# Kernel optimization log

Hardware: AMD Instinct MI355X
Metric: run time of the kernel (lower is better)

## Reference

```python
import jax, jax.numpy as jnp
import numpy as np

H_HEADS = 8
DIM_HEAD = 64
NEG_BIAS = -1.0e9


def setup_inputs() -> dict:
    key = jax.random.key(0)
    ks = jax.random.split(key, 8)
    b, n, l = 4, 4096, 256
    qd, cd = 512, 768
    inner = H_HEADS * DIM_HEAD  # 512
    x = jax.random.normal(ks[0], (b, n, qd), dtype=jnp.float32)
    context = jax.random.normal(ks[1], (b, l, cd), dtype=jnp.float32)
    mask = jax.random.randint(ks[2], (b, l, 128, 128), 0, 2).astype(jnp.int32)
    Wq = jax.random.normal(ks[3], (qd, inner), dtype=jnp.float32) * 0.02
    Wk = jax.random.normal(ks[4], (cd, inner), dtype=jnp.float32) * 0.02
    Wv = jax.random.normal(ks[5], (cd, inner), dtype=jnp.float32) * 0.02
    Wo = jax.random.normal(ks[6], (inner, qd), dtype=jnp.float32) * 0.02
    bo = jnp.zeros((qd,), dtype=jnp.float32)
    return {"x": x, "context": context, "mask": mask,
            "Wq": Wq, "Wk": Wk, "Wv": Wv, "Wo": Wo, "bo": bo}


def _split_heads(t, h):
    # 'b n (h d) -> (b h) n d'
    b, n, hd = t.shape
    d = hd // h
    return t.reshape(b, n, h, d).transpose(0, 2, 1, 3).reshape(b * h, n, d)


def reference(x, context, mask, Wq, Wk, Wv, Wo, bo):
    h = H_HEADS
    scale = DIM_HEAD ** (-0.5)
    b, n, _ = x.shape
    l = context.shape[1]
    size = int(round(n ** 0.5))  # spatial side of the query grid

    q = _split_heads(x @ Wq, h)        # (b*h, n, d)
    k = _split_heads(context @ Wk, h)  # (b*h, l, d)
    v = _split_heads(context @ Wv, h)  # (b*h, l, d)

    sim = jnp.einsum('bid,bjd->bij', q, k) * scale  # (b*h, n, l)

    # F.interpolate(mask, size=size) with default 'nearest': idx = floor(i * H_in / size)
    Hin = mask.shape[2]
    idx = (jnp.arange(size) * Hin) // size
    m = mask[:, :, idx[:, None], idx[None, :]]       # (b, l, size, size)
    m = m.reshape(b, l, n).transpose(0, 2, 1)        # (b, n, l)
    m = jnp.tile(m, (h, 1, 1)).astype(bool)          # (b*h, n, l), tile order as in torch .tile(h,1,1)
    sim = jnp.where(m, sim, sim + NEG_BIAS)

    attn = jax.nn.softmax(sim, axis=-1)
    out = jnp.einsum('bij,bjd->bid', attn, v)        # (b*h, n, d)
    # '(b h) n d -> b n (h d)'
    out = out.reshape(b, h, n, DIM_HEAD).transpose(0, 2, 1, 3).reshape(b, n, h * DIM_HEAD)
    return out @ Wo + bo
```

## Files before the change

kernel.cpp:

```cpp
#include <hip/hip_runtime.h>
#include <hip/hip_bf16.h>

typedef __attribute__((ext_vector_type(8))) short short8;
typedef __attribute__((ext_vector_type(4))) float f32x4;

__device__ __forceinline__ unsigned short f2bf(float f) {
  unsigned int u = __float_as_uint(f);
  u = (u + 0x7FFFu + ((u >> 16) & 1u)) >> 16;
  return (unsigned short)u;
}

__device__ __forceinline__ unsigned int pk2(float a, float b) {
  __hip_bfloat162 h = __float22bfloat162_rn(make_float2(a, b));
  return *reinterpret_cast<unsigned int*>(&h);
}

__device__ __forceinline__ void gl_lds16(const void* g, void* l) {
  __builtin_amdgcn_global_load_lds(
      (const __attribute__((address_space(1))) void*)g,
      (__attribute__((address_space(3))) void*)l, 16, 0, 0);
}

__device__ __forceinline__ void fence_barrier() {
  asm volatile("" ::: "memory");
  __builtin_amdgcn_s_barrier();
  asm volatile("" ::: "memory");
}

__device__ __forceinline__ void store4_bf16(unsigned short* p, int stride,
                                            float v0, float v1, float v2, float v3) {
  unsigned int u01 = pk2(v0, v1), u23 = pk2(v2, v3);
  p[0] = (unsigned short)u01;
  p[stride] = (unsigned short)(u01 >> 16);
  p[2 * stride] = (unsigned short)u23;
  p[3 * stride] = (unsigned short)(u23 >> 16);
}

__global__ void prep_all(const float* __restrict__ Wq, const float* __restrict__ Wk,
                         const float* __restrict__ Wv, const float* __restrict__ Wo,
                         unsigned short* __restrict__ WqT, unsigned short* __restrict__ WkT,
                         unsigned short* __restrict__ WvT, unsigned short* __restrict__ WoT,
                         const int* __restrict__ mask, unsigned char* __restrict__ Mout,
                         const float* __restrict__ x, const float* __restrict__ ctx,
                         unsigned short* __restrict__ xb, unsigned short* __restrict__ ctxb) {
  __shared__ char smem[64 * 256];
  const int bid = blockIdx.x;
  if (bid >= 576) {
    int i = (bid - 576) * 256 + threadIdx.x;
    const float4* src;
    ushort4* dst;
    if (i < 2097152) {
      src = (const float4*)x + i;
      dst = (ushort4*)xb + i;
    } else {
      int j = i - 2097152;
      if (j >= 196608) return;
      src = (const float4*)ctx + j;
      dst = (ushort4*)ctxb + j;
    }
    float4 v = *src;
    ushort4 o;
    o.x = f2bf(v.x); o.y = f2bf(v.y); o.z = f2bf(v.z); o.w = f2bf(v.w);
    *dst = o;
    return;
  }
  if (bid < 320) {
    unsigned short(*t)[65] = (unsigned short(*)[65])smem;
    const float* W; unsigned short* WT; int K, rel;
    float scale = 1.f;
    if (bid < 64)       { W = Wq; WT = WqT; K = 512; rel = bid; scale = 0.125f * 1.4426950408889634f; }
    else if (bid < 160) { W = Wk; WT = WkT; K = 768; rel = bid - 64; }
    else if (bid < 256) { W = Wv; WT = WvT; K = 768; rel = bid - 160; }
    else                { W = Wo; WT = WoT; K = 512; rel = bid - 256; }
    const int N = 512;
    const int tk = rel >> 3, tn = rel & 7;
    const int k0 = tk * 64, n0 = tn * 64;
    const int tt = threadIdx.x;
#pragma unroll
    for (int e = 0; e < 16; ++e) {
      int idx = e * 256 + tt;
      int r = idx >> 6, c = idx & 63;
      t[r][c] = f2bf(scale * W[(size_t)(k0 + r) * N + n0 + c]);
    }
    __syncthreads();
#pragma unroll
    for (int e = 0; e < 16; ++e) {
      int idx = e * 256 + tt;
      int rr = idx & 63, cc = idx >> 6;
      WT[(size_t)(n0 + cc) * K + k0 + rr] = t[rr][cc];
    }
  } else {
    unsigned char* bits = (unsigned char*)smem;
    const int rel = bid - 320;
    const int r2g = rel & 63, bp = rel >> 6;
    const int j = threadIdx.x;
    const int4* row = (const int4*)(mask + ((size_t)(bp * 256 + j) * 128 + r2g * 2) * 128);
#pragma unroll 8
    for (int q = 0; q < 32; ++q) {
      int4 v = row[q];
      bits[(2 * q) * 256 + j] = v.x ? 1 : 0;
      bits[(2 * q + 1) * 256 + j] = v.z ? 1 : 0;
    }
    __syncthreads();
    const int t2 = threadIdx.x;
    const int c = t2 >> 2, ch = t2 & 3;
    uint4* dst = (uint4*)(Mout + ((size_t)bp * 4096 + r2g * 64 + c) * 256 + ch * 64);
#pragma unroll
    for (int q = 0; q < 4; ++q) {
      unsigned int wd[4];
#pragma unroll
      for (int wq = 0; wq < 4; ++wq) {
        unsigned int v = 0;
#pragma unroll
        for (int bb = 0; bb < 4; ++bb) {
          int ob = ch * 64 + q * 16 + wq * 4 + bb;
          int jj = ((ob & 15) << 4) | (ob >> 4);
          v |= ((unsigned int)bits[c * 256 + jj]) << (8 * bb);
        }
        wd[wq] = v;
      }
      uint4 vv; vv.x = wd[0]; vv.y = wd[1]; vv.z = wd[2]; vv.w = wd[3];
      dst[q] = vv;
    }
  }
}

__global__ __launch_bounds__(256, 2) void proj_all(
    const unsigned short* __restrict__ xb, const unsigned short* __restrict__ ctxb,
    const unsigned short* __restrict__ WqT, const unsigned short* __restrict__ WkT,
    const unsigned short* __restrict__ WvT,
    unsigned short* __restrict__ Qb, unsigned short* __restrict__ Kb,
    unsigned short* __restrict__ VTb) {
  __shared__ unsigned short lds_a[2][128 * 64];
  __shared__ unsigned short lds_b[2][128 * 64];
  const int tid = threadIdx.x;
  const int w = tid >> 6, lane = tid & 63;
  const int lo = lane & 15, hi = lane >> 4;
  const int wr = w >> 1, wc = w & 1;
  const int bid = blockIdx.x;
  const int wg = (bid & 7) * 96 + (bid >> 3);

  if (wg < 512) {
    const int m0 = (wg >> 2) * 128, n0 = (wg & 3) * 128;
    const int K = 512;
    f32x4 acc[4][4];
#pragma unroll
    for (int m = 0; m < 4; ++m)
#pragma unroll
      for (int n = 0; n < 4; ++n) acc[m][n] = (f32x4){0.f, 0.f, 0.f, 0.f};

    auto stage = [&](int buf, int k0) {
#pragma unroll
      for (int c = 0; c < 4; ++c) {
        int o = (tid + c * 256) * 16;
        int row = o >> 7, colb = (o & 127) ^ ((row & 7) << 4);
        gl_lds16((const char*)xb + ((size_t)(m0 + row) * K + k0) * 2 + colb,
                 (char*)lds_a[buf] + (w * 64 + c * 256) * 16);
      }
#pragma unroll
      for (int c = 0; c < 4; ++c) {
        int o = (tid + c * 256) * 16;
        int row = o >> 7, colb = (o & 127) ^ ((row & 7) << 4);
        gl_lds16((const char*)WqT + ((size_t)(n0 + row) * K + k0) * 2 + colb,
                 (char*)lds_b[buf] + (w * 64 + c * 256) * 16);
      }
    };

    stage(0, 0);
    int cur = 0;
    for (int t = 0; t < 8; ++t) {
      if (t < 7) {
        stage(cur ^ 1, (t + 1) * 64);
        asm volatile("s_waitcnt vmcnt(8)" ::: "memory");
      } else {
        asm volatile("s_waitcnt vmcnt(0)" ::: "memory");
      }
      fence_barrier();
      short8 a[2][4], b[2][4];
#pragma unroll
      for (int kk = 0; kk < 2; ++kk) {
#pragma unroll
        for (int m = 0; m < 4; ++m) {
          int row = wr * 64 + m * 16 + lo;
          a[kk][m] = *(const short8*)((const char*)lds_a[cur] + row * 128 +
                                      (((kk * 32 + hi * 8) * 2) ^ ((row & 7) << 4)));
        }
#pragma unroll
        for (int n = 0; n < 4; ++n) {
          int row = wc * 64 + n * 16 + lo;
          b[kk][n] = *(const short8*)((const char*)lds_b[cur] + row * 128 +
                                      (((kk * 32 + hi * 8) * 2) ^ ((row & 7) << 4)));
        }
      }
#pragma unroll
      for (int kk = 0; kk < 2; ++kk)
#pragma unroll
        for (int m = 0; m < 4; ++m)
#pragma unroll
          for (int n = 0; n < 4; ++n)
            acc[m][n] = __builtin_amdgcn_mfma_f32_16x16x32_bf16(a[kk][m], b[kk][n], acc[m][n], 0, 0, 0);
      if (t < 7) fence_barrier();
      cur ^= 1;
    }
#pragma unroll
    for (int m = 0; m < 4; ++m)
#pragma unroll
      for (int n = 0; n < 4; ++n) {
        int rbase = m0 + wr * 64 + m * 16 + hi * 4;
        int col = n0 + wc * 64 + n * 16 + lo;
        store4_bf16(&Qb[(size_t)rbase * 512 + col], 512,
                    acc[m][n][0], acc[m][n][1], acc[m][n][2], acc[m][n][3]);
      }
  } else {
    const int rel = wg - 512;
    const int z = rel >> 7, t5 = rel & 127;
    const unsigned short* BT = z ? WvT : WkT;
    const int m0 = (t5 >> 3) * 64, n0 = (t5 & 7) * 64;
    const int K = 768;
    f32x4 acc[2][2];
#pragma unroll
    for (int m = 0; m < 2; ++m)
#pragma unroll
      for (int n = 0; n < 2; ++n) acc[m][n] = (f32x4){0.f, 0.f, 0.f, 0.f};

    auto stage = [&](int buf, int k0) {
#pragma unroll
      for (int c = 0; c < 2; ++c) {
        int o = (tid + c * 256) * 16;
        int row = o >> 7, colb = (o & 127) ^ ((row & 7) << 4);
        gl_lds16((const char*)ctxb + ((size_t)(m0 + row) * K + k0) * 2 + colb,
                 (char*)lds_a[buf] + (w * 64 + c * 256) * 16);
        gl_lds16((const char*)BT + ((size_t)(n0 + row) * K + k0) * 2 + colb,
                 (char*)lds_b[buf] + (w * 64 + c * 256) * 16);
      }
    };

    stage(0, 0);
    int cur = 0;
    for (int t = 0; t < 12; ++t) {
      if (t < 11) {
        stage(cur ^ 1, (t + 1) * 64);
        asm volatile("s_waitcnt vmcnt(4)" ::: "memory");
      } else {
        asm volatile("s_waitcnt vmcnt(0)" ::: "memory");
      }
      fence_barrier();
      short8 a[2][2], b[2][2];
#pragma unroll
      for (int kk = 0; kk < 2; ++kk) {
#pragma unroll
        for (int m = 0; m < 2; ++m) {
          int row = wr * 32 + m * 16 + lo;
          a[kk][m] = *(const short8*)((const char*)lds_a[cur] + row * 128 +
                                      (((kk * 32 + hi * 8) * 2) ^ ((row & 7) << 4)));
        }
#pragma unroll
        for (int n = 0; n < 2; ++n) {
          int row = wc * 32 + n * 16 + lo;
          b[kk][n] = *(const short8*)((const char*)lds_b[cur] + row * 128 +
                                      (((kk * 32 + hi * 8) * 2) ^ ((row & 7) << 4)));
        }
      }
#pragma unroll
      for (int kk = 0; kk < 2; ++kk)
#pragma unroll
        for (int m = 0; m < 2; ++m)
#pragma unroll
          for (int n = 0; n < 2; ++n)
            acc[m][n] = __builtin_amdgcn_mfma_f32_16x16x32_bf16(a[kk][m], b[kk][n], acc[m][n], 0, 0, 0);
      if (t < 11) fence_barrier();
      cur ^= 1;
    }
#pragma unroll
    for (int m = 0; m < 2; ++m)
#pragma unroll
      for (int n = 0; n < 2; ++n) {
        int col = n0 + wc * 32 + n * 16 + lo;
        int rowg = m0 + wr * 32 + m * 16 + hi * 4;
        if (z == 0) {
          store4_bf16(&Kb[(size_t)rowg * 512 + col], 512,
                      acc[m][n][0], acc[m][n][1], acc[m][n][2], acc[m][n][3]);
        } else {
          unsigned int u01 = pk2(acc[m][n][0], acc[m][n][1]);
          unsigned int u23 = pk2(acc[m][n][2], acc[m][n][3]);
          uint2 vv; vv.x = u01; vv.y = u23;
          *(uint2*)&VTb[((size_t)(rowg >> 8) * 512 + col) * 256 + (rowg & 255)] = vv;
        }
      }
  }
}

__global__ void attn_kernel(const unsigned short* __restrict__ Qb,
                            const unsigned short* __restrict__ Kb,
                            const unsigned short* __restrict__ VTb,
                            const unsigned char* __restrict__ Mu8,
                            unsigned short* __restrict__ AOb) {
  __shared__ unsigned short kt[256 * 64];
  __shared__ float rinv_s[64];
  const int tid = threadIdx.x, w = tid >> 6, lane = tid & 63;
  const int lo = lane & 15, hi = lane >> 4;
  const int bid = blockIdx.x;
  const int wg = (bid & 7) * 256 + (bid >> 3);
  const int qt = wg & 63, h = (wg >> 6) & 7, b = wg >> 9;

#pragma unroll
  for (int c = 0; c < 8; ++c) {
    int o = (tid + c * 256) * 16;
    int j = o >> 7, colb = (o & 127) ^ ((j & 7) << 4);
    gl_lds16((const char*)Kb + ((size_t)((b * 256 + j) * 512 + h * 64)) * 2 + colb,
             (char*)kt + (w * 64 + c * 256) * 16);
  }
  short8 qf[2];
  {
    int qrow = qt * 64 + w * 16 + lo;
#pragma unroll
    for (int kk = 0; kk < 2; ++kk)
      qf[kk] = *(const short8*)&Qb[(size_t)(b * 4096 + qrow) * 512 + h * 64 + kk * 32 + hi * 8];
  }
  const unsigned char* mrow = Mu8 + ((size_t)(h & 3) * 4096 + qt * 64 + w * 16) * 256;
  uint4 mv[4];
#pragma unroll
  for (int r = 0; r < 4; ++r)
    mv[r] = *(const uint4*)(mrow + (hi * 4 + r) * 256 + lo * 16);
  __syncthreads();

  f32x4 acc[16];
#pragma unroll
  for (int nt = 0; nt < 16; ++nt) acc[nt] = (f32x4){0.f, 0.f, 0.f, 0.f};
  __builtin_amdgcn_s_setprio(1);
#pragma unroll
  for (int nt = 0; nt < 16; ++nt) {
    int j = nt * 16 + lo;
#pragma unroll
    for (int kk = 0; kk < 2; ++kk) {
      short8 bfr = *(const short8*)((const char*)kt + j * 128 +
                                    (((kk * 32 + hi * 8) * 2) ^ ((j & 7) << 4)));
      acc[nt] = __builtin_amdgcn_mfma_f32_16x16x32_bf16(qf[kk], bfr, acc[nt], 0, 0, 0);
    }
  }
  __builtin_amdgcn_s_setprio(0);

  float rmax[4] = {-3e38f, -3e38f, -3e38f, -3e38f};
#pragma unroll
  for (int nt = 0; nt < 16; ++nt)
#pragma unroll
    for (int r = 0; r < 4; ++r) rmax[r] = fmaxf(rmax[r], acc[nt][r]);
#pragma unroll
  for (int r = 0; r < 4; ++r) {
#pragma unroll
    for (int m2 = 1; m2 < 16; m2 <<= 1)
      rmax[r] = fmaxf(rmax[r], __shfl_xor(rmax[r], m2, 64));
  }
  float rsum[4] = {0.f, 0.f, 0.f, 0.f};
#pragma unroll
  for (int nt = 0; nt < 16; ++nt)
#pragma unroll
    for (int r = 0; r < 4; ++r) {
      unsigned int word = (nt < 4) ? mv[r].x : (nt < 8) ? mv[r].y : (nt < 12) ? mv[r].z : mv[r].w;
      unsigned int mbyte = (word >> ((nt & 3) * 8)) & 0xFFu;
      float p = exp2f(acc[nt][r] - rmax[r]);
      p = mbyte ? p : 0.f;
      acc[nt][r] = p;
      rsum[r] += p;
    }
#pragma unroll
  for (int r = 0; r < 4; ++r) {
#pragma unroll
    for (int m2 = 1; m2 < 16; m2 <<= 1)
      rsum[r] += __shfl_xor(rsum[r], m2, 64);
  }
  if (lo == 0) {
#pragma unroll
    for (int r = 0; r < 4; ++r) rinv_s[w * 16 + hi * 4 + r] = 1.f / rsum[r];
  }

  __syncthreads();

  {
    char* pl = (char*)kt;
    const int q0 = w * 16 + hi * 4;
    const int ro0 = (q0 + 0) * 512, sw0 = ((q0 + 0) & 7) << 4;
    const int ro1 = (q0 + 1) * 512, sw1 = ((q0 + 1) & 7) << 4;
    const int ro2 = (q0 + 2) * 512, sw2 = ((q0 + 2) & 7) << 4;
    const int ro3 = (q0 + 3) * 512, sw3 = ((q0 + 3) & 7) << 4;
#pragma unroll
    for (int nt = 0; nt < 16; ++nt) {
      int j2 = (nt * 16 + lo) * 2;
      unsigned int u01 = pk2(acc[nt][0], acc[nt][1]);
      unsigned int u23 = pk2(acc[nt][2], acc[nt][3]);
      *(unsigned short*)(pl + ro0 + (j2 ^ sw0)) = (unsigned short)u01;
      *(unsigned short*)(pl + ro1 + (j2 ^ sw1)) = (unsigned short)(u01 >> 16);
      *(unsigned short*)(pl + ro2 + (j2 ^ sw2)) = (unsigned short)u23;
      *(unsigned short*)(pl + ro3 + (j2 ^ sw3)) = (unsigned short)(u23 >> 16);
    }
  }
  __syncthreads();

  const int dh = w & 1, qh = w >> 1;
  f32x4 aco[2][2];
#pragma unroll
  for (int m = 0; m < 2; ++m)
#pragma unroll
    for (int n = 0; n < 2; ++n) aco[m][n] = (f32x4){0.f, 0.f, 0.f, 0.f};
  const size_t vbase = ((size_t)b * 512 + h * 64 + dh * 32) * 256;
#pragma unroll
  for (int ks = 0; ks < 8; ++ks) {
    short8 pa[2];
#pragma unroll
    for (int m = 0; m < 2; ++m) {
      int q = qh * 32 + m * 16 + lo;
      pa[m] = *(const short8*)((const char*)kt + q * 512 +
                               (((ks * 32 + hi * 8) * 2) ^ ((q & 7) << 4)));
    }
    __builtin_amdgcn_s_setprio(1);
#pragma unroll
    for (int n = 0; n < 2; ++n) {
      short8 vb = *(const short8*)&VTb[vbase + (size_t)(n * 16 + lo) * 256 + ks * 32 + hi * 8];
#pragma unroll
      for (int m = 0; m < 2; ++m)
        aco[m][n] = __builtin_amdgcn_mfma_f32_16x16x32_bf16(pa[m], vb, aco[m][n], 0, 0, 0);
    }
    __builtin_amdgcn_s_setprio(0);
  }

#pragma unroll
  for (int m = 0; m < 2; ++m) {
    float rv[4];
#pragma unroll
    for (int r = 0; r < 4; ++r) rv[r] = rinv_s[qh * 32 + m * 16 + hi * 4 + r];
#pragma unroll
    for (int n = 0; n < 2; ++n) {
      int col = h * 64 + dh * 32 + n * 16 + lo;
      int rowg = qt * 64 + qh * 32 + m * 16 + hi * 4;
      store4_bf16(&AOb[(size_t)(b * 4096 + rowg) * 512 + col], 512,
                  aco[m][n][0] * rv[0], aco[m][n][1] * rv[1],
                  aco[m][n][2] * rv[2], aco[m][n][3] * rv[3]);
    }
  }
}

__global__ __launch_bounds__(256, 2) void gemm_o(
    const unsigned short* __restrict__ A, const unsigned short* __restrict__ BT,
    float* __restrict__ Cout, const float* __restrict__ bias) {
  __shared__ unsigned short lds_a[2][128 * 64];
  __shared__ unsigned short lds_b[2][128 * 64];
  const int tid = threadIdx.x;
  const int w = tid >> 6, lane = tid & 63;
  const int lo = lane & 15, hi = lane >> 4;
  const int bid = blockIdx.x;
  const int wg = (bid & 7) * 64 + (bid >> 3);
  const int m0 = (wg >> 2) * 128, n0 = (wg & 3) * 128;
  const int wr = w >> 1, wc = w & 1;
  const int K = 512, N = 512;
  f32x4 acc[4][4];
#pragma unroll
  for (int m = 0; m < 4; ++m)
#pragma unroll
    for (int n = 0; n < 4; ++n) acc[m][n] = (f32x4){0.f, 0.f, 0.f, 0.f};

  auto stage = [&](int buf, int k0) {
#pragma unroll
    for (int c = 0; c < 4; ++c) {
      int o = (tid + c * 256) * 16;
      int row = o >> 7, colb = (o & 127) ^ ((row & 7) << 4);
      gl_lds16((const char*)A + ((size_t)(m0 + row) * K + k0) * 2 + colb,
               (char*)lds_a[buf] + (w * 64 + c * 256) * 16);
    }
#pragma unroll
    for (int c = 0; c < 4; ++c) {
      int o = (tid + c * 256) * 16;
      int row = o >> 7, colb = (o & 127) ^ ((row & 7) << 4);
      gl_lds16((const char*)BT + ((size_t)(n0 + row) * K + k0) * 2 + colb,
               (char*)lds_b[buf] + (w * 64 + c * 256) * 16);
    }
  };

  stage(0, 0);
  int cur = 0;
  for (int t = 0; t < 8; ++t) {
    if (t < 7) {
      stage(cur ^ 1, (t + 1) * 64);
      asm volatile("s_waitcnt vmcnt(8)" ::: "memory");
    } else {
      asm volatile("s_waitcnt vmcnt(0)" ::: "memory");
    }
    fence_barrier();
    short8 a[2][4], b[2][4];
#pragma unroll
    for (int kk = 0; kk < 2; ++kk) {
#pragma unroll
      for (int m = 0; m < 4; ++m) {
        int row = wr * 64 + m * 16 + lo;
        a[kk][m] = *(const short8*)((const char*)lds_a[cur] + row * 128 +
                                    (((kk * 32 + hi * 8) * 2) ^ ((row & 7) << 4)));
      }
#pragma unroll
      for (int n = 0; n < 4; ++n) {
        int row = wc * 64 + n * 16 + lo;
        b[kk][n] = *(const short8*)((const char*)lds_b[cur] + row * 128 +
                                    (((kk * 32 + hi * 8) * 2) ^ ((row & 7) << 4)));
      }
    }
#pragma unroll
    for (int kk = 0; kk < 2; ++kk)
#pragma unroll
      for (int m = 0; m < 4; ++m)
#pragma unroll
        for (int n = 0; n < 4; ++n)
          acc[m][n] = __builtin_amdgcn_mfma_f32_16x16x32_bf16(a[kk][m], b[kk][n], acc[m][n], 0, 0, 0);
    if (t < 7) fence_barrier();
    cur ^= 1;
  }

#pragma unroll
  for (int m = 0; m < 4; ++m)
#pragma unroll
    for (int n = 0; n < 4; ++n) {
      int rbase = m0 + wr * 64 + m * 16 + hi * 4;
      int col = n0 + wc * 64 + n * 16 + lo;
#pragma unroll
      for (int r = 0; r < 4; ++r)
        Cout[(size_t)(rbase + r) * N + col] = acc[m][n][r] + bias[col];
    }
}

extern "C" void kernel_launch(void* const* d_in, const int* in_sizes, int n_in,
                              void* d_out, int out_size, void* d_ws, size_t ws_size,
                              hipStream_t stream) {
  const float* x = (const float*)d_in[0];
  const float* ctx = (const float*)d_in[1];
  const int* mask = (const int*)d_in[2];
  const float* Wq = (const float*)d_in[3];
  const float* Wk = (const float*)d_in[4];
  const float* Wv = (const float*)d_in[5];
  const float* Wo = (const float*)d_in[6];
  const float* bo = (const float*)d_in[7];
  float* out = (float*)d_out;

  char* ws = (char*)d_ws;
  size_t off = 0;
  auto alloc = [&](size_t bytes) {
    char* p = ws + off;
    off += (bytes + 255) & ~(size_t)255;
    return p;
  };
  unsigned short* xb   = (unsigned short*)alloc((size_t)16384 * 512 * 2);
  unsigned short* ctxb = (unsigned short*)alloc((size_t)1024 * 768 * 2);
  unsigned short* WqT  = (unsigned short*)alloc((size_t)512 * 512 * 2);
  unsigned short* WkT  = (unsigned short*)alloc((size_t)512 * 768 * 2);
  unsigned short* WvT  = (unsigned short*)alloc((size_t)512 * 768 * 2);
  unsigned short* WoT  = (unsigned short*)alloc((size_t)512 * 512 * 2);
  unsigned short* Qb   = (unsigned short*)alloc((size_t)16384 * 512 * 2);
  unsigned short* Kb   = (unsigned short*)alloc((size_t)1024 * 512 * 2);
  unsigned short* VTb  = (unsigned short*)alloc((size_t)4 * 512 * 256 * 2);
  unsigned short* AOb  = (unsigned short*)alloc((size_t)16384 * 512 * 2);
  unsigned char*  Mu8  = (unsigned char*)alloc((size_t)4 * 4096 * 256);

  prep_all<<<9536, 256, 0, stream>>>(Wq, Wk, Wv, Wo, WqT, WkT, WvT, WoT, mask, Mu8, x, ctx, xb, ctxb);
  proj_all<<<768, 256, 0, stream>>>(xb, ctxb, WqT, WkT, WvT, Qb, Kb, VTb);
  attn_kernel<<<2048, 256, 0, stream>>>(Qb, Kb, VTb, Mu8, AOb);
  gemm_o<<<512, 256, 0, stream>>>(AOb, WoT, out, bo);
}
```

Measured before the change: 82.26 us.

## Make PV stage wave-local with per-wave P buffers, removing block barriers

Each wave now writes its own 16-row slice of the probability matrix into a private LDS buffer in two 128-column halves and immediately multiplies it by V for all 64 head dims. This replaces the shared K-tile reuse, the two block-wide __syncthreads, and the shared rinv array with wave-local waits, and the softmax normalizer is kept in registers. The trade-off is that each wave loads all of V^T for its head from global memory instead of sharing a 32-column slice, which raises global/L2 read traffic, and a separate LDS buffer is added.

```diff
diff --git a/kernel.cpp b/kernel.cpp
--- a/kernel.cpp
+++ b/kernel.cpp
@@ -290,13 +290,12 @@
   }
 }
 
-__global__ void attn_kernel(const unsigned short* __restrict__ Qb,
-                            const unsigned short* __restrict__ Kb,
-                            const unsigned short* __restrict__ VTb,
-                            const unsigned char* __restrict__ Mu8,
-                            unsigned short* __restrict__ AOb) {
+__global__ __launch_bounds__(256) void attn_kernel(
+    const unsigned short* __restrict__ Qb, const unsigned short* __restrict__ Kb,
+    const unsigned short* __restrict__ VTb, const unsigned char* __restrict__ Mu8,
+    unsigned short* __restrict__ AOb) {
   __shared__ unsigned short kt[256 * 64];
-  __shared__ float rinv_s[64];
+  __shared__ unsigned short pt[4][16 * 128];
   const int tid = threadIdx.x, w = tid >> 6, lane = tid & 63;
   const int lo = lane & 15, hi = lane >> 4;
   const int bid = blockIdx.x;
@@ -363,79 +362,57 @@
       acc[nt][r] = p;
       rsum[r] += p;
     }
+  float rinv[4];
 #pragma unroll
   for (int r = 0; r < 4; ++r) {
 #pragma unroll
     for (int m2 = 1; m2 < 16; m2 <<= 1)
       rsum[r] += __shfl_xor(rsum[r], m2, 64);
-  }
-  if (lo == 0) {
-#pragma unroll
-    for (int r = 0; r < 4; ++r) rinv_s[w * 16 + hi * 4 + r] = 1.f / rsum[r];
-  }
-
-  __syncthreads();
-
-  {
-    char* pl = (char*)kt;
-    const int q0 = w * 16 + hi * 4;
-    const int ro0 = (q0 + 0) * 512, sw0 = ((q0 + 0) & 7) << 4;
-    const int ro1 = (q0 + 1) * 512, sw1 = ((q0 + 1) & 7) << 4;
-    const int ro2 = (q0 + 2) * 512, sw2 = ((q0 + 2) & 7) << 4;
-    const int ro3 = (q0 + 3) * 512, sw3 = ((q0 + 3) & 7) << 4;
-#pragma unroll
-    for (int nt = 0; nt < 16; ++nt) {
-      int j2 = (nt * 16 + lo) * 2;
+    rinv[r] = 1.f / rsum[r];
+  }
+
+  char* pw = (char*)(pt[w]);
+  const size_t vbase = ((size_t)b * 512 + h * 64) * 256;
+  f32x4 aco[4];
+#pragma unroll
+  for (int n = 0; n < 4; ++n) aco[n] = (f32x4){0.f, 0.f, 0.f, 0.f};
+#pragma unroll
+  for (int ph = 0; ph < 2; ++ph) {
+    const int q0 = hi * 4;
+#pragma unroll
+    for (int nt2 = 0; nt2 < 8; ++nt2) {
+      int nt = ph * 8 + nt2;
+      int j2 = (nt2 * 16 + lo) * 2;
       unsigned int u01 = pk2(acc[nt][0], acc[nt][1]);
       unsigned int u23 = pk2(acc[nt][2], acc[nt][3]);
-      *(unsigned short*)(pl + ro0 + (j2 ^ sw0)) = (unsigned short)u01;
-      *(unsigned short*)(pl + ro1 + (j2 ^ sw1)) = (unsigned short)(u01 >> 16);
-      *(unsigned short*)(pl + ro2 + (j2 ^ sw2)) = (unsigned short)u23;
-      *(unsigned short*)(pl + ro3 + (j2 ^ sw3)) = (unsigned short)(u23 >> 16);
-    }
-  }
-  __syncthreads();
-
-  const int dh = w & 1, qh = w >> 1;
-  f32x4 aco[2][2];
-#pragma unroll
-  for (int m = 0; m < 2; ++m)
-#pragma unroll
-    for (int n = 0; n < 2; ++n) aco[m][n] = (f32x4){0.f, 0.f, 0.f, 0.f};
-  const size_t vbase = ((size_t)b * 512 + h * 64 + dh * 32) * 256;
-#pragma unroll
-  for (int ks = 0; ks < 8; ++ks) {
-    short8 pa[2];
-#pragma unroll
-    for (int m = 0; m < 2; ++m) {
-      int q = qh * 32 + m * 16 + lo;
-      pa[m] = *(const short8*)((const char*)kt + q * 512 +
-                               (((ks * 32 + hi * 8) * 2) ^ ((q & 7) << 4)));
-    }
-    __builtin_amdgcn_s_setprio(1);
-#pragma unroll
-    for (int n = 0; n < 2; ++n) {
-      short8 vb = *(const short8*)&VTb[vbase + (size_t)(n * 16 + lo) * 256 + ks * 32 + hi * 8];
-#pragma unroll
-      for (int m = 0; m < 2; ++m)
-        aco[m][n] = __builtin_amdgcn_mfma_f32_16x16x32_bf16(pa[m], vb, aco[m][n], 0, 0, 0);
-    }
-    __builtin_amdgcn_s_setprio(0);
-  }
-
-#pragma unroll
-  for (int m = 0; m < 2; ++m) {
-    float rv[4];
-#pragma unroll
-    for (int r = 0; r < 4; ++r) rv[r] = rinv_s[qh * 32 + m * 16 + hi * 4 + r];
-#pragma unroll
-    for (int n = 0; n < 2; ++n) {
-      int col = h * 64 + dh * 32 + n * 16 + lo;
-      int rowg = qt * 64 + qh * 32 + m * 16 + hi * 4;
-      store4_bf16(&AOb[(size_t)(b * 4096 + rowg) * 512 + col], 512,
-                  aco[m][n][0] * rv[0], aco[m][n][1] * rv[1],
-                  aco[m][n][2] * rv[2], aco[m][n][3] * rv[3]);
-    }
+      *(unsigned short*)(pw + (q0 + 0) * 256 + (j2 ^ (((q0 + 0) & 7) << 4))) = (unsigned short)u01;
+      *(unsigned short*)(pw + (q0 + 1) * 256 + (j2 ^ (((q0 + 1) & 7) << 4))) = (unsigned short)(u01 >> 16);
+      *(unsigned short*)(pw + (q0 + 2) * 256 + (j2 ^ (((q0 + 2) & 7) << 4))) = (unsigned short)u23;
+      *(unsigned short*)(pw + (q0 + 3) * 256 + (j2 ^ (((q0 + 3) & 7) << 4))) = (unsigned short)(u23 >> 16);
+    }
+    asm volatile("s_waitcnt lgkmcnt(0)" ::: "memory");
+    __builtin_amdgcn_sched_barrier(0);
+#pragma unroll
+    for (int ks = 0; ks < 4; ++ks) {
+      short8 pa = *(const short8*)(pw + lo * 256 + (((ks * 32 + hi * 8) * 2) ^ ((lo & 7) << 4)));
+      __builtin_amdgcn_s_setprio(1);
+#pragma unroll
+      for (int n = 0; n < 4; ++n) {
+        short8 vb = *(const short8*)&VTb[vbase + (size_t)(n * 16 + lo) * 256 +
+                                         ph * 128 + ks * 32 + hi * 8];
+        aco[n] = __builtin_amdgcn_mfma_f32_16x16x32_bf16(pa, vb, aco[n], 0, 0, 0);
+      }
+      __builtin_amdgcn_s_setprio(0);
+    }
+  }
+
+#pragma unroll
+  for (int n = 0; n < 4; ++n) {
+    int col = h * 64 + n * 16 + lo;
+    int rowg = qt * 64 + w * 16 + hi * 4;
+    store4_bf16(&AOb[(size_t)(b * 4096 + rowg) * 512 + col], 512,
+                aco[n][0] * rinv[0], aco[n][1] * rinv[1],
+                aco[n][2] * rinv[2], aco[n][3] * rinv[3]);
   }
 }
 
```

Result: slower. 101.9 us (+23.9%).
